# Performance work log

Measured on AMD Instinct MI355X. Metric: run time of the kernel, lower is better.

## Reference

```python
import jax, jax.numpy as jnp
import numpy as np

IN_DIM = 135909   # input feature vocab (Amazon-670K style)
OUT_DIM = 670091  # output classes
D = 128           # hardcoded embedding dim in the module
B = 256           # batch size
T = 100           # active features per sample (summed bag-of-features)


def setup_inputs() -> dict:
    key = jax.random.key(0)
    ks = jax.random.split(key, 6)
    x = jax.random.randint(ks[0], (B, T), 0, IN_DIM)
    y = jax.random.randint(ks[1], (B,), 0, OUT_DIM)
    # nn.Embedding(IN+1, 128, padding_idx=IN): last row is the zero padding row
    emb_table = jax.random.normal(ks[2], (IN_DIM + 1, D), jnp.float32) * 0.01
    emb_table = emb_table.at[IN_DIM].set(0.0)
    stdv = 1.0 / np.sqrt(IN_DIM)
    bias = jax.random.uniform(ks[3], (D,), jnp.float32, -stdv, stdv)
    # LSHSoftmax dense parameters: per-class weight [OUT, D] and bias [OUT]
    W = jax.random.normal(ks[4], (OUT_DIM, D), jnp.float32) * (1.0 / np.sqrt(D))
    b_out = jnp.zeros((OUT_DIM,), jnp.float32)
    return {"x": x, "y": y, "freeze": 0, "slide": 0,
            "emb_table": emb_table, "bias": bias, "W": W, "b_out": b_out}


def reference(x, y, freeze, slide, emb_table, bias, W, b_out):
    # raw_emb = sum over the feature indices (bag-of-features embedding sum)
    raw = jnp.sum(emb_table[x], axis=1)                      # [B, D]
    emb = raw / jnp.linalg.norm(raw, axis=1, keepdims=True)  # L2 normalize
    query = jax.nn.relu(emb + bias)                          # [B, D]
    # LSHSoftmax exact (slide=0 / full) path: dense softmax cross-entropy
    logits = query @ W.T + b_out                             # [B, OUT]
    logp = jax.nn.log_softmax(logits, axis=-1)
    loss = -jnp.mean(jnp.take_along_axis(logp, y[:, None], axis=1))
    return loss
```

## Files before the change

### kernel.cpp

```cpp
#include <hip/hip_runtime.h>
#include <hip/hip_bf16.h>

#define IN_DIMX 135909
#define OUT_DIMX 670091
#define DDIM 128
#define BATCH 256
#define TFEAT 100
#define NBLK 512
#define NCHUNK ((OUT_DIMX + 63) / 64)

typedef __bf16 bf16_t;
typedef __attribute__((ext_vector_type(8))) __bf16 bf16x8;
typedef __attribute__((ext_vector_type(4))) __bf16 bf16x4;
typedef __attribute__((ext_vector_type(4))) float f32x4;

__global__ void k_query(const int* __restrict__ x, const float* __restrict__ emb,
                        const float* __restrict__ bias, float* __restrict__ qf,
                        bf16_t* __restrict__ qb) {
    const int row = blockIdx.x;
    const int t = threadIdx.x;
    __shared__ int sidx[TFEAT];
    if (t < TFEAT) sidx[t] = x[row * TFEAT + t];
    __syncthreads();
    float s = 0.f;
    #pragma unroll 10
    for (int i = 0; i < TFEAT; ++i) {
        s += emb[(size_t)sidx[i] * DDIM + t];
    }
    float sq = s * s;
    #pragma unroll
    for (int off = 1; off < 64; off <<= 1) sq += __shfl_xor(sq, off, 64);
    __shared__ float wred[2];
    if ((threadIdx.x & 63) == 0) wred[threadIdx.x >> 6] = sq;
    __syncthreads();
    const float tot = wred[0] + wred[1];
    float q = s / sqrtf(tot) + bias[t];
    q = fmaxf(q, 0.f);
    qf[row * DDIM + t] = q;
    qb[row * DDIM + t] = (bf16_t)q;
}

__global__ __launch_bounds__(256, 2)
void k_lse(const float* __restrict__ W, const float* __restrict__ b_out,
           const bf16_t* __restrict__ qb, float* __restrict__ partials) {
    __shared__ bf16_t lds[2][64 * DDIM];
    const int tid = threadIdx.x;
    const int lane = tid & 63;
    const int w = tid >> 6;
    const int l15 = lane & 15;
    const int l4 = lane >> 4;

    bf16x8 a[4][4];
    #pragma unroll
    for (int mt = 0; mt < 4; ++mt)
        #pragma unroll
        for (int ks = 0; ks < 4; ++ks)
            a[mt][ks] = *(const bf16x8*)(qb + (w * 64 + mt * 16 + l15) * DDIM + ks * 32 + 8 * l4);

    float rs[4][4];
    #pragma unroll
    for (int mt = 0; mt < 4; ++mt)
        #pragma unroll
        for (int r = 0; r < 4; ++r) rs[mt][r] = 0.f;

    const int srow = tid >> 5;
    const int scol = (tid & 31) * 4;
    const int c16  = (tid & 31) >> 1;
    const int half = (tid & 1) * 4;

    f32x4 wr[8];
    float bo_n[4];

    auto issue = [&](int ch) {
        const int cb = ch * 64;
        #pragma unroll
        for (int j = 0; j < 8; ++j) {
            int r = cb + j * 8 + srow;
            r = (r < OUT_DIMX) ? r : 0;
            wr[j] = *(const f32x4*)(W + (size_t)r * DDIM + scol);
        }
        #pragma unroll
        for (int nt = 0; nt < 4; ++nt) {
            int c = cb + nt * 16 + l15;
            c = (c < OUT_DIMX) ? c : 0;
            bo_n[nt] = b_out[c];
        }
    };

    auto convwrite = [&](int cur) {
        #pragma unroll
        for (int j = 0; j < 8; ++j) {
            const int row = j * 8 + srow;
            const int sp = row * 16 + (c16 ^ (row & 7));
            bf16x4 v;
            v[0] = (bf16_t)wr[j][0]; v[1] = (bf16_t)wr[j][1];
            v[2] = (bf16_t)wr[j][2]; v[3] = (bf16_t)wr[j][3];
            *(bf16x4*)(&lds[cur][sp * 8 + half]) = v;
        }
    };

    int cur = 0;
    issue(blockIdx.x);
    for (int ch = blockIdx.x; ch < NCHUNK; ch += NBLK) {
        float bo_c[4];
        #pragma unroll
        for (int nt = 0; nt < 4; ++nt) bo_c[nt] = bo_n[nt];

        convwrite(cur);
        __syncthreads();
        __builtin_amdgcn_sched_barrier(0);
        if (ch + NBLK < NCHUNK) issue(ch + NBLK);

        f32x4 acc[4][4];
        #pragma unroll
        for (int mt = 0; mt < 4; ++mt)
            #pragma unroll
            for (int nt = 0; nt < 4; ++nt) acc[mt][nt] = (f32x4){0.f, 0.f, 0.f, 0.f};

        #pragma unroll
        for (int ks = 0; ks < 4; ++ks) {
            bf16x8 b[4];
            #pragma unroll
            for (int nt = 0; nt < 4; ++nt) {
                const int row = nt * 16 + l15;
                const int sp = row * 16 + ((ks * 4 + l4) ^ (row & 7));
                b[nt] = *(const bf16x8*)(&lds[cur][sp * 8]);
            }
            #pragma unroll
            for (int nt = 0; nt < 4; ++nt)
                #pragma unroll
                for (int mt = 0; mt < 4; ++mt)
                    acc[mt][nt] = __builtin_amdgcn_mfma_f32_16x16x32_bf16(
                        a[mt][ks], b[nt], acc[mt][nt], 0, 0, 0);
        }

        const int cbase = ch * 64;
        if (cbase + 64 <= OUT_DIMX) {
            #pragma unroll
            for (int nt = 0; nt < 4; ++nt)
                #pragma unroll
                for (int mt = 0; mt < 4; ++mt)
                    #pragma unroll
                    for (int r = 0; r < 4; ++r)
                        rs[mt][r] += __expf(acc[mt][nt][r] + bo_c[nt]);
        } else {
            #pragma unroll
            for (int nt = 0; nt < 4; ++nt) {
                const bool valid = (cbase + nt * 16 + l15 < OUT_DIMX);
                #pragma unroll
                for (int mt = 0; mt < 4; ++mt)
                    #pragma unroll
                    for (int r = 0; r < 4; ++r)
                        rs[mt][r] += valid ? __expf(acc[mt][nt][r] + bo_c[nt]) : 0.f;
            }
        }
        cur ^= 1;
    }

    #pragma unroll
    for (int mt = 0; mt < 4; ++mt)
        #pragma unroll
        for (int r = 0; r < 4; ++r) {
            float v = rs[mt][r];
            v += __shfl_xor(v, 1, 64);
            v += __shfl_xor(v, 2, 64);
            v += __shfl_xor(v, 4, 64);
            v += __shfl_xor(v, 8, 64);
            if (l15 == 0) {
                const int rowb = w * 64 + mt * 16 + l4 * 4 + r;
                partials[(size_t)rowb * NBLK + blockIdx.x] = v;
            }
        }
}

__global__ void k_ydot(const int* __restrict__ y, const float* __restrict__ qf,
                       const float* __restrict__ W, const float* __restrict__ b_out,
                       float* __restrict__ logity) {
    const int i = blockIdx.x;
    const int lane = threadIdx.x;
    const int yi = y[i];
    const float* wrow = W + (size_t)yi * DDIM;
    const float* qrow = qf + i * DDIM;
    float s = qrow[lane] * wrow[lane] + qrow[lane + 64] * wrow[lane + 64];
    #pragma unroll
    for (int off = 1; off < 64; off <<= 1) s += __shfl_xor(s, off, 64);
    if (lane == 0) logity[i] = s + b_out[yi];
}

__global__ void k_rowlse(const float* __restrict__ partials,
                         const float* __restrict__ logity,
                         float* __restrict__ rowloss) {
    const int i = blockIdx.x;
    const int lane = threadIdx.x;
    float s = 0.f;
    #pragma unroll
    for (int k = 0; k < NBLK / 64; ++k)
        s += partials[(size_t)i * NBLK + k * 64 + lane];
    #pragma unroll
    for (int off = 1; off < 64; off <<= 1) s += __shfl_xor(s, off, 64);
    if (lane == 0) rowloss[i] = logf(s) - logity[i];
}

__global__ void k_final(const float* __restrict__ rowloss, float* __restrict__ out) {
    const int i = threadIdx.x;
    float t = rowloss[i];
    #pragma unroll
    for (int off = 1; off < 64; off <<= 1) t += __shfl_xor(t, off, 64);
    __shared__ float wred[4];
    if ((threadIdx.x & 63) == 0) wred[threadIdx.x >> 6] = t;
    __syncthreads();
    if (threadIdx.x == 0)
        out[0] = (wred[0] + wred[1] + wred[2] + wred[3]) * (1.0f / (float)BATCH);
}

extern "C" void kernel_launch(void* const* d_in, const int* in_sizes, int n_in,
                              void* d_out, int out_size, void* d_ws, size_t ws_size,
                              hipStream_t stream) {
    const int*   x     = (const int*)d_in[0];
    const int*   y     = (const int*)d_in[1];
    const float* emb   = (const float*)d_in[4];
    const float* bias  = (const float*)d_in[5];
    const float* W     = (const float*)d_in[6];
    const float* b_out = (const float*)d_in[7];
    float* out = (float*)d_out;

    char* ws = (char*)d_ws;
    bf16_t* qb       = (bf16_t*)(ws);
    float*  qf       = (float*)(ws + 65536);
    float*  logity   = (float*)(ws + 196608);
    float*  rowloss  = (float*)(ws + 197632);
    float*  partials = (float*)(ws + 262144);

    k_query<<<BATCH, DDIM, 0, stream>>>(x, emb, bias, qf, qb);
    k_ydot<<<BATCH, 64, 0, stream>>>(y, qf, W, b_out, logity);
    k_lse<<<NBLK, 256, 0, stream>>>(W, b_out, qb, partials);
    k_rowlse<<<BATCH, 64, 0, stream>>>(partials, logity, rowloss);
    k_final<<<1, 256, 0, stream>>>(rowloss, out);
}
```

Measured before the change: 90.65 us.

## Raise lse occupancy, shrink accumulators, use exp2, fuse ydot into rowlse

Restructures the MFMA loop so each column tile's accumulators are computed and consumed before the next, cutting live accumulator registers. This allows launch bounds of 3 blocks per SM and a larger grid of 768 blocks. The exponent becomes exp2 with the bias prescaled by log2e. The separate target-logit kernel is folded into the row reduction kernel, removing one launch. The trade-off is less MFMA interleaving across tiles within a chunk.

```diff
diff --git a/kernel.cpp b/kernel.cpp
--- a/kernel.cpp
+++ b/kernel.cpp
@@ -6,8 +6,9 @@
 #define DDIM 128
 #define BATCH 256
 #define TFEAT 100
-#define NBLK 512
+#define NBLK 768
 #define NCHUNK ((OUT_DIMX + 63) / 64)
+#define LOG2E 1.44269504088896f
 
 typedef __bf16 bf16_t;
 typedef __attribute__((ext_vector_type(8))) __bf16 bf16x8;
@@ -40,7 +41,7 @@
     qb[row * DDIM + t] = (bf16_t)q;
 }
 
-__global__ __launch_bounds__(256, 2)
+__global__ __launch_bounds__(256, 3)
 void k_lse(const float* __restrict__ W, const float* __restrict__ b_out,
            const bf16_t* __restrict__ qb, float* __restrict__ partials) {
     __shared__ bf16_t lds[2][64 * DDIM];
@@ -81,9 +82,9 @@
         }
         #pragma unroll
         for (int nt = 0; nt < 4; ++nt) {
-            int c = cb + nt * 16 + l15;
-            c = (c < OUT_DIMX) ? c : 0;
-            bo_n[nt] = b_out[c];
+            int cc = cb + nt * 16 + l15;
+            cc = (cc < OUT_DIMX) ? cc : 0;
+            bo_n[nt] = b_out[cc] * LOG2E;
         }
     };
 
@@ -111,47 +112,51 @@
         __builtin_amdgcn_sched_barrier(0);
         if (ch + NBLK < NCHUNK) issue(ch + NBLK);
 
-        f32x4 acc[4][4];
-        #pragma unroll
-        for (int mt = 0; mt < 4; ++mt)
-            #pragma unroll
-            for (int nt = 0; nt < 4; ++nt) acc[mt][nt] = (f32x4){0.f, 0.f, 0.f, 0.f};
-
-        #pragma unroll
-        for (int ks = 0; ks < 4; ++ks) {
-            bf16x8 b[4];
-            #pragma unroll
-            for (int nt = 0; nt < 4; ++nt) {
-                const int row = nt * 16 + l15;
-                const int sp = row * 16 + ((ks * 4 + l4) ^ (row & 7));
-                b[nt] = *(const bf16x8*)(&lds[cur][sp * 8]);
-            }
-            #pragma unroll
-            for (int nt = 0; nt < 4; ++nt)
-                #pragma unroll
-                for (int mt = 0; mt < 4; ++mt)
-                    acc[mt][nt] = __builtin_amdgcn_mfma_f32_16x16x32_bf16(
-                        a[mt][ks], b[nt], acc[mt][nt], 0, 0, 0);
-        }
-
         const int cbase = ch * 64;
         if (cbase + 64 <= OUT_DIMX) {
             #pragma unroll
-            for (int nt = 0; nt < 4; ++nt)
+            for (int nt = 0; nt < 4; ++nt) {
+                f32x4 acc[4];
+                #pragma unroll
+                for (int mt = 0; mt < 4; ++mt) acc[mt] = (f32x4){0.f, 0.f, 0.f, 0.f};
+                const int row = nt * 16 + l15;
+                #pragma unroll
+                for (int ks = 0; ks < 4; ++ks) {
+                    const int sp = row * 16 + ((ks * 4 + l4) ^ (row & 7));
+                    const bf16x8 b = *(const bf16x8*)(&lds[cur][sp * 8]);
+                    #pragma unroll
+                    for (int mt = 0; mt < 4; ++mt)
+                        acc[mt] = __builtin_amdgcn_mfma_f32_16x16x32_bf16(
+                            a[mt][ks], b, acc[mt], 0, 0, 0);
+                }
                 #pragma unroll
                 for (int mt = 0; mt < 4; ++mt)
                     #pragma unroll
                     for (int r = 0; r < 4; ++r)
-                        rs[mt][r] += __expf(acc[mt][nt][r] + bo_c[nt]);
+                        rs[mt][r] += exp2f(fmaf(acc[mt][r], LOG2E, bo_c[nt]));
+            }
         } else {
             #pragma unroll
             for (int nt = 0; nt < 4; ++nt) {
+                f32x4 acc[4];
+                #pragma unroll
+                for (int mt = 0; mt < 4; ++mt) acc[mt] = (f32x4){0.f, 0.f, 0.f, 0.f};
+                const int row = nt * 16 + l15;
+                #pragma unroll
+                for (int ks = 0; ks < 4; ++ks) {
+                    const int sp = row * 16 + ((ks * 4 + l4) ^ (row & 7));
+                    const bf16x8 b = *(const bf16x8*)(&lds[cur][sp * 8]);
+                    #pragma unroll
+                    for (int mt = 0; mt < 4; ++mt)
+                        acc[mt] = __builtin_amdgcn_mfma_f32_16x16x32_bf16(
+                            a[mt][ks], b, acc[mt], 0, 0, 0);
+                }
                 const bool valid = (cbase + nt * 16 + l15 < OUT_DIMX);
                 #pragma unroll
                 for (int mt = 0; mt < 4; ++mt)
                     #pragma unroll
                     for (int r = 0; r < 4; ++r)
-                        rs[mt][r] += valid ? __expf(acc[mt][nt][r] + bo_c[nt]) : 0.f;
+                        rs[mt][r] += valid ? exp2f(fmaf(acc[mt][r], LOG2E, bo_c[nt])) : 0.f;
             }
         }
         cur ^= 1;
@@ -173,22 +178,11 @@
         }
 }
 
-__global__ void k_ydot(const int* __restrict__ y, const float* __restrict__ qf,
-                       const float* __restrict__ W, const float* __restrict__ b_out,
-                       float* __restrict__ logity) {
-    const int i = blockIdx.x;
-    const int lane = threadIdx.x;
-    const int yi = y[i];
-    const float* wrow = W + (size_t)yi * DDIM;
-    const float* qrow = qf + i * DDIM;
-    float s = qrow[lane] * wrow[lane] + qrow[lane + 64] * wrow[lane + 64];
-    #pragma unroll
-    for (int off = 1; off < 64; off <<= 1) s += __shfl_xor(s, off, 64);
-    if (lane == 0) logity[i] = s + b_out[yi];
-}
-
 __global__ void k_rowlse(const float* __restrict__ partials,
-                         const float* __restrict__ logity,
+                         const int* __restrict__ y,
+                         const float* __restrict__ qf,
+                         const float* __restrict__ W,
+                         const float* __restrict__ b_out,
                          float* __restrict__ rowloss) {
     const int i = blockIdx.x;
     const int lane = threadIdx.x;
@@ -196,9 +190,16 @@
     #pragma unroll
     for (int k = 0; k < NBLK / 64; ++k)
         s += partials[(size_t)i * NBLK + k * 64 + lane];
-    #pragma unroll
-    for (int off = 1; off < 64; off <<= 1) s += __shfl_xor(s, off, 64);
-    if (lane == 0) rowloss[i] = logf(s) - logity[i];
+    const int yi = y[i];
+    const float* wrow = W + (size_t)yi * DDIM;
+    const float* qrow = qf + i * DDIM;
+    float d = qrow[lane] * wrow[lane] + qrow[lane + 64] * wrow[lane + 64];
+    #pragma unroll
+    for (int off = 1; off < 64; off <<= 1) {
+        s += __shfl_xor(s, off, 64);
+        d += __shfl_xor(d, off, 64);
+    }
+    if (lane == 0) rowloss[i] = logf(s) - (d + b_out[yi]);
 }
 
 __global__ void k_final(const float* __restrict__ rowloss, float* __restrict__ out) {
@@ -227,13 +228,11 @@
     char* ws = (char*)d_ws;
     bf16_t* qb       = (bf16_t*)(ws);
     float*  qf       = (float*)(ws + 65536);
-    float*  logity   = (float*)(ws + 196608);
     float*  rowloss  = (float*)(ws + 197632);
     float*  partials = (float*)(ws + 262144);
 
     k_query<<<BATCH, DDIM, 0, stream>>>(x, emb, bias, qf, qb);
-    k_ydot<<<BATCH, 64, 0, stream>>>(y, qf, W, b_out, logity);
     k_lse<<<NBLK, 256, 0, stream>>>(W, b_out, qb, partials);
-    k_rowlse<<<BATCH, 64, 0, stream>>>(partials, logity, rowloss);
+    k_rowlse<<<BATCH, 64, 0, stream>>>(partials, y, qf, W, b_out, rowloss);
     k_final<<<1, 256, 0, stream>>>(rowloss, out);
 }
```

New measurement: 189.6 us. 2.09x slower.
